# Performance work log

Measured on AMD Instinct MI355X. Metric: run time of the kernel, lower is better.

The kernel has to match this reference:

```python
import jax, jax.numpy as jnp
import numpy as np

DIM = 1024
N_HEADS = 16
HEAD_DIM = DIM // N_HEADS
D_LATENT = 256
B, T = 1, 4096


def setup_inputs() -> dict:
    key = jax.random.key(0)
    ks = jax.random.split(key, 6)
    s = 0.02
    return {
        "x": jax.random.normal(ks[0], (B, T, DIM), dtype=jnp.float32),
        "W_DKV": jax.random.normal(ks[1], (DIM, D_LATENT), dtype=jnp.float32) * s,
        "W_UK": jax.random.normal(ks[2], (D_LATENT, DIM), dtype=jnp.float32) * s,
        "W_UV": jax.random.normal(ks[3], (D_LATENT, DIM), dtype=jnp.float32) * s,
        "W_UQ": jax.random.normal(ks[4], (DIM, DIM), dtype=jnp.float32) * s,
        "W_O": jax.random.normal(ks[5], (DIM, DIM), dtype=jnp.float32) * s,
    }


def reference(x, W_DKV, W_UK, W_UV, W_UQ, W_O):
    b, t, d = x.shape
    h, hd = N_HEADS, HEAD_DIM
    # low-rank latent KV projection
    c_kv = x @ W_DKV                                   # (b, t, d_latent)
    k = (c_kv @ W_UK).reshape(b, t, h, hd)             # (b, t, h, hd)
    v = (c_kv @ W_UV).reshape(b, t, h, hd)
    q = (x @ W_UQ).reshape(b, t, h, hd)
    scale = 1.0 / jnp.sqrt(jnp.asarray(hd, x.dtype))
    scores = jnp.einsum("bqhd,bkhd->bhqk", q, k) * scale   # (b, h, t, t)
    causal = jnp.tril(jnp.ones((t, t), dtype=bool))
    scores = jnp.where(causal, scores, jnp.asarray(-jnp.inf, scores.dtype))
    probs = jax.nn.softmax(scores, axis=-1)            # dropout is eval-mode identity
    ctx = jnp.einsum("bhqk,bkhd->bqhd", probs, v).reshape(b, t, d)
    return ctx @ W_O
```

## Files before the change

### kernel.cpp

```cpp
#include <hip/hip_runtime.h>
#include <hip/hip_bf16.h>
#include <stdint.h>

#define T_SEQ 4096
#define DIMX 1024
#define NH 16
#define HD 64
#define DLAT 256

typedef __bf16 bf16x8 __attribute__((ext_vector_type(8)));
typedef float floatx4 __attribute__((ext_vector_type(4)));

#define MFMA(a, b, c) __builtin_amdgcn_mfma_f32_16x16x32_bf16(a, b, c, 0, 0, 0)

__device__ inline void gload_lds16(const __bf16* g, __bf16* l) {
  __builtin_amdgcn_global_load_lds(
      (const __attribute__((address_space(1))) uint32_t*)g,
      (__attribute__((address_space(3))) uint32_t*)l, 16, 0, 0);
}

__global__ __launch_bounds__(256) void prep_kernel(
    const float* __restrict__ x, const float* __restrict__ wdkv,
    const float* __restrict__ wuk, const float* __restrict__ wuv,
    const float* __restrict__ wuq, const float* __restrict__ wo,
    __bf16* __restrict__ x_bf, __bf16* __restrict__ wt_dkv,
    __bf16* __restrict__ wt_uk, __bf16* __restrict__ wt_uv,
    __bf16* __restrict__ wt_uq, __bf16* __restrict__ wt_o) {
  int id = blockIdx.x;
  if (id < 2048) {
    int i = id * 256 + threadIdx.x;
    const float4* p = (const float4*)x;
    float4 a = p[2 * i], b = p[2 * i + 1];
    bf16x8 r = {(__bf16)a.x, (__bf16)a.y, (__bf16)a.z, (__bf16)a.w,
                (__bf16)b.x, (__bf16)b.y, (__bf16)b.z, (__bf16)b.w};
    *(bf16x8*)(x_bf + 8 * (size_t)i) = r;
    return;
  }
  int t = id - 2048;
  const float* in;
  __bf16* out;
  int R, C, lt;
  if (t < 64)       { in = wdkv; out = wt_dkv; R = 1024; C = 256;  lt = t; }
  else if (t < 128) { in = wuk;  out = wt_uk;  R = 256;  C = 1024; lt = t - 64; }
  else if (t < 192) { in = wuv;  out = wt_uv;  R = 256;  C = 1024; lt = t - 128; }
  else if (t < 448) { in = wuq;  out = wt_uq;  R = 1024; C = 1024; lt = t - 192; }
  else              { in = wo;   out = wt_o;   R = 1024; C = 1024; lt = t - 448; }
  __shared__ __bf16 tls[64][65];
  int tpr = C >> 6;
  int r0 = (lt / tpr) * 64, c0 = (lt % tpr) * 64;
  int tid = threadIdx.x;
#pragma unroll
  for (int i = 0; i < 16; i++) {
    int idx = tid + i * 256;
    int r = idx >> 6, c = idx & 63;
    tls[r][c] = (__bf16)in[(size_t)(r0 + r) * C + c0 + c];
  }
  __syncthreads();
#pragma unroll
  for (int i = 0; i < 16; i++) {
    int idx = tid + i * 256;
    int rr = idx & 63, cc = idx >> 6;
    out[(size_t)(c0 + cc) * R + r0 + rr] = tls[rr][cc];
  }
}


__global__ __launch_bounds__(256) void gemm_a128(const __bf16* __restrict__ A,
                                                 const __bf16* __restrict__ B1,
                                                 const __bf16* __restrict__ B2,
                                                 __bf16* __restrict__ C1,
                                                 __bf16* __restrict__ C2) {
  __shared__ __attribute__((aligned(16))) __bf16 Al[128 * 32];
  __shared__ __attribute__((aligned(16))) __bf16 Bl[128 * 32];
  int tid = threadIdx.x;
  int w = tid >> 6, lane = tid & 63;
  int quad = lane >> 4, l16 = lane & 15;
  int mw = w & 1, nw = w >> 1;
  int bx = blockIdx.x, m0 = blockIdx.y * 128;
  const __bf16* Bt;
  __bf16* C;
  int n0, N;
  float sc;
  if (bx < 2) { Bt = B1; C = C1; n0 = bx * 128; N = DLAT; sc = 1.0f; }
  else        { Bt = B2; C = C2; n0 = (bx - 2) * 128; N = DIMX; sc = 0.125f; }
  const int K = DIMX;
  int arow = w * 32 + (lane >> 2), acol = (lane & 3) << 3;

  floatx4 acc[4][4];
#pragma unroll
  for (int i = 0; i < 4; i++)
#pragma unroll
    for (int j = 0; j < 4; j++) acc[i][j] = (floatx4){0.f, 0.f, 0.f, 0.f};

  for (int k0 = 0; k0 < K; k0 += 32) {
#pragma unroll
    for (int j = 0; j < 2; j++) {
      gload_lds16(A + (size_t)(m0 + arow + j * 16) * K + k0 + acol,
                  &Al[(w * 32 + j * 16) * 32]);
      gload_lds16(Bt + (size_t)(n0 + arow + j * 16) * K + k0 + acol,
                  &Bl[(w * 32 + j * 16) * 32]);
    }
    __syncthreads();
    bf16x8 af[4], bfr[4];
#pragma unroll
    for (int mt = 0; mt < 4; mt++)
      af[mt] = *(const bf16x8*)&Al[(mw * 64 + mt * 16 + l16) * 32 + quad * 8];
#pragma unroll
    for (int nt = 0; nt < 4; nt++)
      bfr[nt] = *(const bf16x8*)&Bl[(nw * 64 + nt * 16 + l16) * 32 + quad * 8];
#pragma unroll
    for (int mt = 0; mt < 4; mt++)
#pragma unroll
      for (int nt = 0; nt < 4; nt++)
        acc[mt][nt] = MFMA(af[mt], bfr[nt], acc[mt][nt]);
    __syncthreads();
  }
#pragma unroll
  for (int mt = 0; mt < 4; mt++)
#pragma unroll
    for (int nt = 0; nt < 4; nt++)
#pragma unroll
      for (int r = 0; r < 4; r++) {
        int row = m0 + mw * 64 + mt * 16 + quad * 4 + r;
        int col = n0 + nw * 64 + nt * 16 + l16;
        C[(size_t)row * N + col] = (__bf16)(acc[mt][nt][r] * sc);
      }
}

__global__ __launch_bounds__(256) void gemm_kv128(const __bf16* __restrict__ A,
                                                  const __bf16* __restrict__ Bk,
                                                  const __bf16* __restrict__ Bv,
                                                  __bf16* __restrict__ k,
                                                  __bf16* __restrict__ vt) {
  __shared__ __attribute__((aligned(16))) __bf16 Al[128 * 32];
  __shared__ __attribute__((aligned(16))) __bf16 Bl[128 * 32];
  __shared__ __attribute__((aligned(16))) __bf16 tw[4][64 * 72];
  int tid = threadIdx.x;
  int w = tid >> 6, lane = tid & 63;
  int quad = lane >> 4, l16 = lane & 15;
  int mw = w & 1, nw = w >> 1;
  int bx = blockIdx.x, m0 = blockIdx.y * 128;
  bool is_k = (bx < 8);
  const __bf16* Bt = is_k ? Bk : Bv;
  int n0 = (is_k ? bx : bx - 8) * 128;
  const int K = DLAT;
  int arow = w * 32 + (lane >> 2), acol = (lane & 3) << 3;

  floatx4 acc[4][4];
#pragma unroll
  for (int i = 0; i < 4; i++)
#pragma unroll
    for (int j = 0; j < 4; j++) acc[i][j] = (floatx4){0.f, 0.f, 0.f, 0.f};

  for (int k0 = 0; k0 < K; k0 += 32) {
#pragma unroll
    for (int j = 0; j < 2; j++) {
      gload_lds16(A + (size_t)(m0 + arow + j * 16) * K + k0 + acol,
                  &Al[(w * 32 + j * 16) * 32]);
      gload_lds16(Bt + (size_t)(n0 + arow + j * 16) * K + k0 + acol,
                  &Bl[(w * 32 + j * 16) * 32]);
    }
    __syncthreads();
    bf16x8 af[4], bfr[4];
#pragma unroll
    for (int mt = 0; mt < 4; mt++)
      af[mt] = *(const bf16x8*)&Al[(mw * 64 + mt * 16 + l16) * 32 + quad * 8];
#pragma unroll
    for (int nt = 0; nt < 4; nt++)
      bfr[nt] = *(const bf16x8*)&Bl[(nw * 64 + nt * 16 + l16) * 32 + quad * 8];
#pragma unroll
    for (int mt = 0; mt < 4; mt++)
#pragma unroll
      for (int nt = 0; nt < 4; nt++)
        acc[mt][nt] = MFMA(af[mt], bfr[nt], acc[mt][nt]);
    __syncthreads();
  }
  if (is_k) {
#pragma unroll
    for (int mt = 0; mt < 4; mt++)
#pragma unroll
      for (int nt = 0; nt < 4; nt++)
#pragma unroll
        for (int r = 0; r < 4; r++) {
          int row = m0 + mw * 64 + mt * 16 + quad * 4 + r;
          int col = n0 + nw * 64 + nt * 16 + l16;
          k[(size_t)row * DIMX + col] = (__bf16)acc[mt][nt][r];
        }
  } else {
#pragma unroll
    for (int mt = 0; mt < 4; mt++)
#pragma unroll
      for (int nt = 0; nt < 4; nt++)
#pragma unroll
        for (int r = 0; r < 4; r++)
          tw[w][(nt * 16 + l16) * 72 + mt * 16 + quad * 4 + r] =
              (__bf16)acc[mt][nt][r];
    int cbase = lane >> 3, chunk = lane & 7;
#pragma unroll
    for (int i = 0; i < 8; i++) {
      int c = cbase + i * 8;
      bf16x8 v8 = *(const bf16x8*)&tw[w][c * 72 + chunk * 8];
      *(bf16x8*)&vt[(size_t)(n0 + nw * 64 + c) * T_SEQ + m0 + mw * 64 +
                    chunk * 8] = v8;
    }
  }
}

__global__ __launch_bounds__(256) void gemm_f128(const __bf16* __restrict__ A,
                                                 const __bf16* __restrict__ Bt,
                                                 float* __restrict__ C) {
  __shared__ __attribute__((aligned(16))) __bf16 Al[128 * 32];
  __shared__ __attribute__((aligned(16))) __bf16 Bl[128 * 32];
  int tid = threadIdx.x;
  int w = tid >> 6, lane = tid & 63;
  int quad = lane >> 4, l16 = lane & 15;
  int mw = w & 1, nw = w >> 1;
  int n0 = blockIdx.x * 128, m0 = blockIdx.y * 128;
  const int K = DIMX, N = DIMX;
  int arow = w * 32 + (lane >> 2), acol = (lane & 3) << 3;

  floatx4 acc[4][4];
#pragma unroll
  for (int i = 0; i < 4; i++)
#pragma unroll
    for (int j = 0; j < 4; j++) acc[i][j] = (floatx4){0.f, 0.f, 0.f, 0.f};

  for (int k0 = 0; k0 < K; k0 += 32) {
#pragma unroll
    for (int j = 0; j < 2; j++) {
      gload_lds16(A + (size_t)(m0 + arow + j * 16) * K + k0 + acol,
                  &Al[(w * 32 + j * 16) * 32]);
      gload_lds16(Bt + (size_t)(n0 + arow + j * 16) * K + k0 + acol,
                  &Bl[(w * 32 + j * 16) * 32]);
    }
    __syncthreads();
    bf16x8 af[4], bfr[4];
#pragma unroll
    for (int mt = 0; mt < 4; mt++)
      af[mt] = *(const bf16x8*)&Al[(mw * 64 + mt * 16 + l16) * 32 + quad * 8];
#pragma unroll
    for (int nt = 0; nt < 4; nt++)
      bfr[nt] = *(const bf16x8*)&Bl[(nw * 64 + nt * 16 + l16) * 32 + quad * 8];
#pragma unroll
    for (int mt = 0; mt < 4; mt++)
#pragma unroll
      for (int nt = 0; nt < 4; nt++)
        acc[mt][nt] = MFMA(af[mt], bfr[nt], acc[mt][nt]);
    __syncthreads();
  }
#pragma unroll
  for (int mt = 0; mt < 4; mt++)
#pragma unroll
    for (int nt = 0; nt < 4; nt++)
#pragma unroll
      for (int r = 0; r < 4; r++) {
        int row = m0 + mw * 64 + mt * 16 + quad * 4 + r;
        int col = n0 + nw * 64 + nt * 16 + l16;
        C[(size_t)row * N + col] = acc[mt][nt][r];
      }
}

#define PST 72
__global__ __launch_bounds__(512, 4) void mla_attn5(const __bf16* __restrict__ Q,
                                                    const __bf16* __restrict__ Kg,
                                                    const __bf16* __restrict__ Vt,
                                                    __bf16* __restrict__ ctx) {
  __shared__ __attribute__((aligned(16))) __bf16 Kl[2][64 * 64];
  __shared__ __attribute__((aligned(16))) __bf16 Vl[2][64 * 64];
  __shared__ __attribute__((aligned(16))) __bf16 Pl[128 * PST];
  int tid = threadIdx.x;
  int wave = tid >> 6, lane = tid & 63;
  int quad = lane >> 4, l16 = lane & 15;
  int wq = wave & 3;
  bool isA = (wave < 4);
  int h = blockIdx.y;
  int qa = (h & 8) ? (31 - blockIdx.x) : blockIdx.x;
  int qb = 63 - qa;
  int myqt = isA ? qa : qb;
  int myq0 = myqt * 64;
  int srow = tid >> 3, pos = tid & 7;
  int gco = pos << 3;
  int sw = ((pos ^ (srow & 7)) << 3);
  int swr = srow * 64 + sw;

  *(bf16x8*)&Pl[srow * PST + gco] =
      *(const bf16x8*)&Q[(size_t)(qa * 64 + srow) * DIMX + h * HD + gco];
  *(bf16x8*)&Pl[(64 + srow) * PST + gco] =
      *(const bf16x8*)&Q[(size_t)(qb * 64 + srow) * DIMX + h * HD + gco];
  *(bf16x8*)&Kl[0][swr] =
      *(const bf16x8*)&Kg[(size_t)srow * DIMX + h * HD + gco];
  *(bf16x8*)&Vl[0][swr] =
      *(const bf16x8*)&Vt[(size_t)(h * HD + srow) * T_SEQ + gco];
  __syncthreads();
  int fr = (wave * 16 + l16) * PST;
  bf16x8 qf0 = *(const bf16x8*)&Pl[fr + quad * 8];
  bf16x8 qf1 = *(const bf16x8*)&Pl[fr + 32 + quad * 8];

  int c0s = ((quad ^ (l16 & 7)) << 3);
  int c1s = (((4 + quad) ^ (l16 & 7)) << 3);

  floatx4 o[4];
  float l_i[4];
#pragma unroll
  for (int i = 0; i < 4; i++) {
    o[i] = (floatx4){0.f, 0.f, 0.f, 0.f};
    l_i[i] = 0.f;
  }

  for (int kt = 0; kt <= qb; kt++) {
    int cur = kt & 1, nxt = cur ^ 1;
    bool pre = (kt < qb);
    bf16x8 kpre, vpre;
    if (pre) {
      int k0n = (kt + 1) * 64;
      kpre = *(const bf16x8*)&Kg[(size_t)(k0n + srow) * DIMX + h * HD + gco];
      vpre = *(const bf16x8*)&Vt[(size_t)(h * HD + srow) * T_SEQ + k0n + gco];
    }
    if (!isA || kt <= qa) {
      const __bf16* Kc = Kl[cur];
      const __bf16* Vc = Vl[cur];
      floatx4 s[4];
#pragma unroll
      for (int ct = 0; ct < 4; ct++) {
        int rb = (ct * 16 + l16) * 64;
        bf16x8 kf0 = *(const bf16x8*)&Kc[rb + c0s];
        bf16x8 kf1 = *(const bf16x8*)&Kc[rb + c1s];
        floatx4 z = (floatx4){0.f, 0.f, 0.f, 0.f};
        z = MFMA(qf0, kf0, z);
        z = MFMA(qf1, kf1, z);
        s[ct] = z;
      }
      bool diag = (kt == myqt);
#pragma unroll
      for (int ct = 0; ct < 4; ct++)
#pragma unroll
        for (int r = 0; r < 4; r++) {
          float p = __expf(s[ct][r]);
          if (diag && (ct * 16 + l16 > wq * 16 + quad * 4 + r)) p = 0.f;
          l_i[r] += p;
          Pl[(wave * 16 + quad * 4 + r) * PST + ct * 16 + l16] = (__bf16)p;
        }
      bf16x8 pf0 = *(const bf16x8*)&Pl[fr + quad * 8];
      bf16x8 pf1 = *(const bf16x8*)&Pl[fr + 32 + quad * 8];
#pragma unroll
      for (int dt = 0; dt < 4; dt++) {
        int rb = (dt * 16 + l16) * 64;
        bf16x8 vf0 = *(const bf16x8*)&Vc[rb + c0s];
        bf16x8 vf1 = *(const bf16x8*)&Vc[rb + c1s];
        o[dt] = MFMA(pf0, vf0, o[dt]);
        o[dt] = MFMA(pf1, vf1, o[dt]);
      }
    }
    if (pre) {
      *(bf16x8*)&Kl[nxt][swr] = kpre;
      *(bf16x8*)&Vl[nxt][swr] = vpre;
    }
    __syncthreads();
  }

#pragma unroll
  for (int off = 1; off < 16; off <<= 1)
#pragma unroll
    for (int r = 0; r < 4; r++) l_i[r] += __shfl_xor(l_i[r], off, 64);

#pragma unroll
  for (int dt = 0; dt < 4; dt++)
#pragma unroll
    for (int r = 0; r < 4; r++) {
      float val = o[dt][r] / l_i[r];
      int row = myq0 + wq * 16 + quad * 4 + r;
      int col = h * HD + dt * 16 + l16;
      ctx[(size_t)row * DIMX + col] = (__bf16)val;
    }
}

extern "C" void kernel_launch(void* const* d_in, const int* in_sizes, int n_in,
                              void* d_out, int out_size, void* d_ws,
                              size_t ws_size, hipStream_t stream) {
  const float* x = (const float*)d_in[0];
  const float* wdkv = (const float*)d_in[1];
  const float* wuk = (const float*)d_in[2];
  const float* wuv = (const float*)d_in[3];
  const float* wuq = (const float*)d_in[4];
  const float* wo = (const float*)d_in[5];
  float* out = (float*)d_out;

  __bf16* ws = (__bf16*)d_ws;
  __bf16* x_bf = ws;
  __bf16* q = x_bf + (size_t)T_SEQ * DIMX;
  __bf16* k = q + (size_t)T_SEQ * DIMX;
  __bf16* vt = k + (size_t)T_SEQ * DIMX;
  __bf16* ctx = vt + (size_t)T_SEQ * DIMX;
  __bf16* ckv = ctx + (size_t)T_SEQ * DIMX;
  __bf16* wt_dkv = ckv + (size_t)T_SEQ * DLAT;
  __bf16* wt_uk = wt_dkv + (size_t)DLAT * DIMX;
  __bf16* wt_uv = wt_uk + (size_t)DIMX * DLAT;
  __bf16* wt_uq = wt_uv + (size_t)DIMX * DLAT;
  __bf16* wt_o = wt_uq + (size_t)DIMX * DIMX;

  dim3 blk(256);
  prep_kernel<<<dim3(2752), blk, 0, stream>>>(x, wdkv, wuk, wuv, wuq, wo, x_bf,
                                              wt_dkv, wt_uk, wt_uv, wt_uq, wt_o);
  gemm_a128<<<dim3(10, T_SEQ / 128), blk, 0, stream>>>(x_bf, wt_dkv, wt_uq,
                                                       ckv, q);
  gemm_kv128<<<dim3(16, T_SEQ / 128), blk, 0, stream>>>(ckv, wt_uk, wt_uv, k,
                                                        vt);
  mla_attn5<<<dim3(32, NH), dim3(512), 0, stream>>>(q, k, vt, ctx);
  gemm_f128<<<dim3(DIMX / 128, T_SEQ / 128), blk, 0, stream>>>(ctx, wt_o, out);
}
```

Measured before the change: 214.1 us.

## Halve attention block to 4 waves, each computing 32 query rows

New measurement: 228.8 us. 6.9% more time.

```diff
diff --git a/kernel.cpp b/kernel.cpp
--- a/kernel.cpp
+++ b/kernel.cpp
@@ -63,7 +63,6 @@
     out[(size_t)(c0 + cc) * R + r0 + rr] = tls[rr][cc];
   }
 }
-
 
 __global__ __launch_bounds__(256) void gemm_a128(const __bf16* __restrict__ A,
                                                  const __bf16* __restrict__ B1,
@@ -261,7 +260,7 @@
 }
 
 #define PST 72
-__global__ __launch_bounds__(512, 4) void mla_attn5(const __bf16* __restrict__ Q,
+__global__ __launch_bounds__(256, 2) void mla_attn6(const __bf16* __restrict__ Q,
                                                     const __bf16* __restrict__ Kg,
                                                     const __bf16* __restrict__ Vt,
                                                     __bf16* __restrict__ ctx) {
@@ -269,91 +268,122 @@
   __shared__ __attribute__((aligned(16))) __bf16 Vl[2][64 * 64];
   __shared__ __attribute__((aligned(16))) __bf16 Pl[128 * PST];
   int tid = threadIdx.x;
-  int wave = tid >> 6, lane = tid & 63;
+  int w = tid >> 6, lane = tid & 63;
   int quad = lane >> 4, l16 = lane & 15;
-  int wq = wave & 3;
-  bool isA = (wave < 4);
+  int tile = w >> 1, half = w & 1;
   int h = blockIdx.y;
   int qa = (h & 8) ? (31 - blockIdx.x) : blockIdx.x;
   int qb = 63 - qa;
-  int myqt = isA ? qa : qb;
-  int myq0 = myqt * 64;
+  int myqt = tile ? qb : qa;
+  int pbase = tile * 64 + half * 32;
   int srow = tid >> 3, pos = tid & 7;
   int gco = pos << 3;
-  int sw = ((pos ^ (srow & 7)) << 3);
-  int swr = srow * 64 + sw;
-
-  *(bf16x8*)&Pl[srow * PST + gco] =
-      *(const bf16x8*)&Q[(size_t)(qa * 64 + srow) * DIMX + h * HD + gco];
-  *(bf16x8*)&Pl[(64 + srow) * PST + gco] =
-      *(const bf16x8*)&Q[(size_t)(qb * 64 + srow) * DIMX + h * HD + gco];
-  *(bf16x8*)&Kl[0][swr] =
-      *(const bf16x8*)&Kg[(size_t)srow * DIMX + h * HD + gco];
-  *(bf16x8*)&Vl[0][swr] =
-      *(const bf16x8*)&Vt[(size_t)(h * HD + srow) * T_SEQ + gco];
+  int sw = (pos ^ (srow & 7)) << 3;
+
+#pragma unroll
+  for (int i = 0; i < 4; i++) {
+    int prow = srow + i * 32;
+    int grow = (i < 2 ? qa : qb) * 64 + srow + (i & 1) * 32;
+    *(bf16x8*)&Pl[prow * PST + gco] =
+        *(const bf16x8*)&Q[(size_t)grow * DIMX + h * HD + gco];
+  }
+#pragma unroll
+  for (int i = 0; i < 2; i++) {
+    int r = srow + i * 32;
+    int a = r * 64 + sw;
+    *(bf16x8*)&Kl[0][a] = *(const bf16x8*)&Kg[(size_t)r * DIMX + h * HD + gco];
+    *(bf16x8*)&Vl[0][a] = *(const bf16x8*)&Vt[(size_t)(h * HD + r) * T_SEQ + gco];
+  }
   __syncthreads();
-  int fr = (wave * 16 + l16) * PST;
-  bf16x8 qf0 = *(const bf16x8*)&Pl[fr + quad * 8];
-  bf16x8 qf1 = *(const bf16x8*)&Pl[fr + 32 + quad * 8];
-
-  int c0s = ((quad ^ (l16 & 7)) << 3);
-  int c1s = (((4 + quad) ^ (l16 & 7)) << 3);
-
-  floatx4 o[4];
-  float l_i[4];
-#pragma unroll
-  for (int i = 0; i < 4; i++) {
-    o[i] = (floatx4){0.f, 0.f, 0.f, 0.f};
-    l_i[i] = 0.f;
-  }
+  bf16x8 qf[2][2];
+#pragma unroll
+  for (int rt = 0; rt < 2; rt++)
+#pragma unroll
+    for (int kh = 0; kh < 2; kh++)
+      qf[rt][kh] = *(const bf16x8*)&Pl[(pbase + rt * 16 + l16) * PST + kh * 32 +
+                                       quad * 8];
+
+  floatx4 o[2][4];
+  float l_i[2][4];
+#pragma unroll
+  for (int rt = 0; rt < 2; rt++)
+#pragma unroll
+    for (int i = 0; i < 4; i++) {
+      o[rt][i] = (floatx4){0.f, 0.f, 0.f, 0.f};
+      l_i[rt][i] = 0.f;
+    }
 
   for (int kt = 0; kt <= qb; kt++) {
     int cur = kt & 1, nxt = cur ^ 1;
     bool pre = (kt < qb);
-    bf16x8 kpre, vpre;
+    bf16x8 kpre[2], vpre[2];
     if (pre) {
       int k0n = (kt + 1) * 64;
-      kpre = *(const bf16x8*)&Kg[(size_t)(k0n + srow) * DIMX + h * HD + gco];
-      vpre = *(const bf16x8*)&Vt[(size_t)(h * HD + srow) * T_SEQ + k0n + gco];
-    }
-    if (!isA || kt <= qa) {
+#pragma unroll
+      for (int i = 0; i < 2; i++) {
+        int r = srow + i * 32;
+        kpre[i] = *(const bf16x8*)&Kg[(size_t)(k0n + r) * DIMX + h * HD + gco];
+        vpre[i] = *(const bf16x8*)&Vt[(size_t)(h * HD + r) * T_SEQ + k0n + gco];
+      }
+    }
+    if (tile || kt <= qa) {
       const __bf16* Kc = Kl[cur];
       const __bf16* Vc = Vl[cur];
-      floatx4 s[4];
+      floatx4 s[2][4];
 #pragma unroll
       for (int ct = 0; ct < 4; ct++) {
         int rb = (ct * 16 + l16) * 64;
-        bf16x8 kf0 = *(const bf16x8*)&Kc[rb + c0s];
-        bf16x8 kf1 = *(const bf16x8*)&Kc[rb + c1s];
-        floatx4 z = (floatx4){0.f, 0.f, 0.f, 0.f};
-        z = MFMA(qf0, kf0, z);
-        z = MFMA(qf1, kf1, z);
-        s[ct] = z;
+        bf16x8 kf0 = *(const bf16x8*)&Kc[rb + ((quad ^ (l16 & 7)) << 3)];
+        bf16x8 kf1 = *(const bf16x8*)&Kc[rb + (((4 + quad) ^ (l16 & 7)) << 3)];
+#pragma unroll
+        for (int rt = 0; rt < 2; rt++) {
+          floatx4 z = (floatx4){0.f, 0.f, 0.f, 0.f};
+          z = MFMA(qf[rt][0], kf0, z);
+          z = MFMA(qf[rt][1], kf1, z);
+          s[rt][ct] = z;
+        }
       }
       bool diag = (kt == myqt);
 #pragma unroll
-      for (int ct = 0; ct < 4; ct++)
-#pragma unroll
-        for (int r = 0; r < 4; r++) {
-          float p = __expf(s[ct][r]);
-          if (diag && (ct * 16 + l16 > wq * 16 + quad * 4 + r)) p = 0.f;
-          l_i[r] += p;
-          Pl[(wave * 16 + quad * 4 + r) * PST + ct * 16 + l16] = (__bf16)p;
-        }
-      bf16x8 pf0 = *(const bf16x8*)&Pl[fr + quad * 8];
-      bf16x8 pf1 = *(const bf16x8*)&Pl[fr + 32 + quad * 8];
+      for (int rt = 0; rt < 2; rt++)
+#pragma unroll
+        for (int ct = 0; ct < 4; ct++)
+#pragma unroll
+          for (int r = 0; r < 4; r++) {
+            float p = __expf(s[rt][ct][r]);
+            if (diag &&
+                (ct * 16 + l16 > half * 32 + rt * 16 + quad * 4 + r))
+              p = 0.f;
+            l_i[rt][r] += p;
+            Pl[(pbase + rt * 16 + quad * 4 + r) * PST + ct * 16 + l16] =
+                (__bf16)p;
+          }
+      bf16x8 pf[2][2];
+#pragma unroll
+      for (int rt = 0; rt < 2; rt++)
+#pragma unroll
+        for (int kh = 0; kh < 2; kh++)
+          pf[rt][kh] = *(const bf16x8*)&Pl[(pbase + rt * 16 + l16) * PST +
+                                           kh * 32 + quad * 8];
 #pragma unroll
       for (int dt = 0; dt < 4; dt++) {
         int rb = (dt * 16 + l16) * 64;
-        bf16x8 vf0 = *(const bf16x8*)&Vc[rb + c0s];
-        bf16x8 vf1 = *(const bf16x8*)&Vc[rb + c1s];
-        o[dt] = MFMA(pf0, vf0, o[dt]);
-        o[dt] = MFMA(pf1, vf1, o[dt]);
+        bf16x8 vf0 = *(const bf16x8*)&Vc[rb + ((quad ^ (l16 & 7)) << 3)];
+        bf16x8 vf1 = *(const bf16x8*)&Vc[rb + (((4 + quad) ^ (l16 & 7)) << 3)];
+#pragma unroll
+        for (int rt = 0; rt < 2; rt++) {
+          o[rt][dt] = MFMA(pf[rt][0], vf0, o[rt][dt]);
+          o[rt][dt] = MFMA(pf[rt][1], vf1, o[rt][dt]);
+        }
       }
     }
     if (pre) {
-      *(bf16x8*)&Kl[nxt][swr] = kpre;
-      *(bf16x8*)&Vl[nxt][swr] = vpre;
+#pragma unroll
+      for (int i = 0; i < 2; i++) {
+        int a = (srow + i * 32) * 64 + sw;
+        *(bf16x8*)&Kl[nxt][a] = kpre[i];
+        *(bf16x8*)&Vl[nxt][a] = vpre[i];
+      }
     }
     __syncthreads();
   }
@@ -361,17 +391,22 @@
 #pragma unroll
   for (int off = 1; off < 16; off <<= 1)
 #pragma unroll
-    for (int r = 0; r < 4; r++) l_i[r] += __shfl_xor(l_i[r], off, 64);
-
-#pragma unroll
-  for (int dt = 0; dt < 4; dt++)
-#pragma unroll
-    for (int r = 0; r < 4; r++) {
-      float val = o[dt][r] / l_i[r];
-      int row = myq0 + wq * 16 + quad * 4 + r;
-      int col = h * HD + dt * 16 + l16;
-      ctx[(size_t)row * DIMX + col] = (__bf16)val;
-    }
+    for (int rt = 0; rt < 2; rt++)
+#pragma unroll
+      for (int r = 0; r < 4; r++)
+        l_i[rt][r] += __shfl_xor(l_i[rt][r], off, 64);
+
+#pragma unroll
+  for (int rt = 0; rt < 2; rt++)
+#pragma unroll
+    for (int dt = 0; dt < 4; dt++)
+#pragma unroll
+      for (int r = 0; r < 4; r++) {
+        float val = o[rt][dt][r] / l_i[rt][r];
+        int row = myqt * 64 + half * 32 + rt * 16 + quad * 4 + r;
+        int col = h * HD + dt * 16 + l16;
+        ctx[(size_t)row * DIMX + col] = (__bf16)val;
+      }
 }
 
 extern "C" void kernel_launch(void* const* d_in, const int* in_sizes, int n_in,
@@ -405,6 +440,6 @@
                                                        ckv, q);
   gemm_kv128<<<dim3(16, T_SEQ / 128), blk, 0, stream>>>(ckv, wt_uk, wt_uv, k,
                                                         vt);
-  mla_attn5<<<dim3(32, NH), dim3(512), 0, stream>>>(q, k, vt, ctx);
+  mla_attn6<<<dim3(32, NH), blk, 0, stream>>>(q, k, vt, ctx);
   gemm_f128<<<dim3(DIMX / 128, T_SEQ / 128), blk, 0, stream>>>(ctx, wt_o, out);
 }
```
